# Optimization experiments

Hardware: AMD Instinct MI355X
Metric: run time of the kernel (lower is better)

The kernel has to match this reference:

```python
import jax, jax.numpy as jnp
import numpy as np

ROUTING_ITERS = 3
EPS = 1e-8


def squash(x):
    # scale = ||x||^2 / (1 + ||x||^2); out = scale * x / (||x|| + eps)
    norm = jnp.linalg.norm(x, axis=-1, keepdims=True)
    scale = norm ** 2 / (1.0 + norm ** 2)
    return scale * x / (norm + EPS)


def setup_inputs() -> dict:
    key = jax.random.key(0)
    kx, kw = jax.random.split(key)
    B, R, C, IC, OC = 256, 1152, 10, 8, 16
    x = jax.random.normal(kx, (B, R, IC), dtype=jnp.float32)
    # learned prediction weights: [1, num_routes, num_capsules, in_ch, out_ch]
    weights = jax.random.normal(kw, (1, R, C, IC, OC), dtype=jnp.float32)
    return {"x": x, "weights": weights}


def reference(x, weights):
    # prediction vectors u_hat[b,r,c,o] = sum_i x[b,r,i] * W[r,c,i,o]
    u = jnp.einsum('bri,rcio->brco', x, weights[0])  # [B,R,C,OC]
    b = jnp.zeros(u.shape[:3], dtype=u.dtype)        # routing logits [B,R,C]
    v = jnp.zeros(u.shape[:1] + u.shape[2:], dtype=u.dtype)
    for _ in range(ROUTING_ITERS):
        c = jax.nn.softmax(b, axis=-1)               # coupling coeffs over capsules
        s = jnp.einsum('brc,brco->bco', c, u)        # weighted sum over routes
        v = squash(s)                                # [B,C,OC]
        b = b + jnp.einsum('brco,bco->brc', u, v)    # agreement update
    return v
```

## Files before the change

kernel.cpp:

```cpp
#include <hip/hip_runtime.h>
#include <cstdint>
#include <cstddef>

#define NB 256
#define NR 1152
#define NC 10
#define NI 8
#define NO 16
#define NSPLIT 2
#define NSWEEP 9
#define NRC 144

static __device__ __forceinline__ uint32_t bf16_pack2(float lo, float hi) {
    uint32_t vl = __float_as_uint(lo);
    vl = vl + 0x7FFFu + ((vl >> 16) & 1u);
    uint32_t vh = __float_as_uint(hi);
    vh = vh + 0x7FFFu + ((vh >> 16) & 1u);
    return (vl >> 16) | (vh & 0xFFFF0000u);
}

__global__ __launch_bounds__(320) void caps_u_s1_kernel(
    const float* __restrict__ x, const float* __restrict__ W,
    uint32_t* __restrict__ u, uint32_t* __restrict__ part1)
{
    const int t  = threadIdx.x;
    const int c  = t >> 5;
    const int rl = (t & 31) >> 2;
    const int oq = t & 3;
    const int rc = blockIdx.x >> 4;
    const int bg = blockIdx.x & 15;
    const int b0 = bg * 16;
    const int r  = rc * 8 + rl;

    __shared__ float xs[16][8][8];

    if (t < 256) {
        const int bi = t >> 4, rem = t & 15;
        const int rr = rem >> 1, hf = rem & 1;
        *(float4*)&xs[bi][rr][hf * 4] =
            *(const float4*)(x + ((size_t)(b0 + bi) * NR + rc * 8 + rr) * 8 + hf * 4);
    }

    const float* wb = W + ((size_t)r * NC + c) * (NI * NO) + oq * 4;
    float4 wf[8];
#pragma unroll
    for (int i = 0; i < 8; ++i) wf[i] = *(const float4*)(wb + i * NO);

    __syncthreads();

#pragma unroll 2
    for (int bi = 0; bi < 16; ++bi) {
        const float4 xv4a = *(const float4*)&xs[bi][rl][0];
        const float4 xv4b = *(const float4*)&xs[bi][rl][4];
        const float xr[8] = {xv4a.x, xv4a.y, xv4a.z, xv4a.w,
                             xv4b.x, xv4b.y, xv4b.z, xv4b.w};
        float ax = 0.f, ay = 0.f, az = 0.f, aw = 0.f;
#pragma unroll
        for (int i = 0; i < 8; ++i) {
            const float xv = xr[i];
            ax = fmaf(xv, wf[i].x, ax); ay = fmaf(xv, wf[i].y, ay);
            az = fmaf(xv, wf[i].z, az); aw = fmaf(xv, wf[i].w, aw);
        }
        uint2 s;
        s.x = bf16_pack2(ax, ay);
        s.y = bf16_pack2(az, aw);
        *(uint2*)(u + (((size_t)(b0 + bi) * NC + c) * NR + r) * 8 + oq * 2) = s;

        float sx = ax, sy = ay, sz = az, sw = aw;
#pragma unroll
        for (int off = 4; off <= 16; off <<= 1) {
            sx += __shfl_xor(sx, off); sy += __shfl_xor(sy, off);
            sz += __shfl_xor(sz, off); sw += __shfl_xor(sw, off);
        }
        if ((t & 28) == 0) {
            uint2 p;
            p.x = bf16_pack2(sx, sy);
            p.y = bf16_pack2(sz, sw);
            *(uint2*)(part1 + ((size_t)(b0 + bi) * NRC + rc) * 80
                      + c * 8 + oq * 2) = p;
        }
    }
}

__global__ __launch_bounds__(192) void caps_s1_reduce_kernel(
    const uint32_t* __restrict__ part1, float* __restrict__ vsum)
{
    const int b = blockIdx.x;
    const int t = threadIdx.x;
    if (t >= 160) return;
    const uint32_t* p = part1 + (size_t)b * NRC * 80 + (t >> 1);
    const bool hi = t & 1;
    float s0 = 0.f, s1 = 0.f, s2 = 0.f, s3 = 0.f;
#pragma unroll 4
    for (int g = 0; g < NRC; g += 4) {
        const uint32_t w0 = p[(g + 0) * 80];
        const uint32_t w1 = p[(g + 1) * 80];
        const uint32_t w2 = p[(g + 2) * 80];
        const uint32_t w3 = p[(g + 3) * 80];
        s0 += hi ? __uint_as_float(w0 & 0xFFFF0000u) : __uint_as_float(w0 << 16);
        s1 += hi ? __uint_as_float(w1 & 0xFFFF0000u) : __uint_as_float(w1 << 16);
        s2 += hi ? __uint_as_float(w2 & 0xFFFF0000u) : __uint_as_float(w2 << 16);
        s3 += hi ? __uint_as_float(w3 & 0xFFFF0000u) : __uint_as_float(w3 << 16);
    }
    const float s = 0.1f * ((s0 + s1) + (s2 + s3));
    float n2 = s * s;
    n2 += __shfl_xor(n2, 1);
    n2 += __shfl_xor(n2, 2);
    n2 += __shfl_xor(n2, 4);
    n2 += __shfl_xor(n2, 8);
    const float nrm = sqrtf(n2);
    vsum[(size_t)b * 160 + t] = s * (n2 / (1.f + n2) / (nrm + 1e-8f));
}

__global__ __launch_bounds__(256, 2) void caps_pass_kernel(
    const uint32_t* __restrict__ u, const float* __restrict__ vsum,
    const float* __restrict__ part_prev, float* __restrict__ partout)
{
    const int b  = blockIdx.x >> 1;
    const int sp = blockIdx.x & 1;
    const int t  = threadIdx.x;
    const int oq = t & 3;
    const int rl = t >> 2;

    __shared__ float vss[160];
    __shared__ float sred[4][160];

    if (t < 160) {
        float v = vsum[(size_t)b * 160 + t];
        if (part_prev != nullptr) {
            const float s = part_prev[(size_t)b * 160 + t]
                          + part_prev[((size_t)NB + b) * 160 + t];
            float n2 = s * s;
            n2 += __shfl_xor(n2, 1);
            n2 += __shfl_xor(n2, 2);
            n2 += __shfl_xor(n2, 4);
            n2 += __shfl_xor(n2, 8);
            const float nrm = sqrtf(n2);
            v += s * (n2 / (1.f + n2) / (nrm + 1e-8f));
        }
        vss[t] = v;
    }
    __syncthreads();

    float acc[10][4];
#pragma unroll
    for (int c = 0; c < 10; ++c)
#pragma unroll
        for (int j = 0; j < 4; ++j) acc[c][j] = 0.f;

    const uint2* ub = (const uint2*)u + (size_t)b * NC * NR * 4 + oq;

    for (int k = 0; k < NSWEEP; ++k) {
        const int r = sp * (NSWEEP * 64) + k * 64 + rl;
        uint2 q[10];
#pragma unroll
        for (int c = 0; c < 10; ++c) q[c] = ub[((size_t)c * NR + r) * 4];

        float lg[10];
#pragma unroll
        for (int c = 0; c < 10; ++c) {
            const float4 vq = *(const float4*)&vss[c * 16 + oq * 4];
            float d = __uint_as_float(q[c].x << 16) * vq.x;
            d = fmaf(__uint_as_float(q[c].x & 0xFFFF0000u), vq.y, d);
            d = fmaf(__uint_as_float(q[c].y << 16),         vq.z, d);
            d = fmaf(__uint_as_float(q[c].y & 0xFFFF0000u), vq.w, d);
            lg[c] = d;
        }
#pragma unroll
        for (int c = 0; c < 10; ++c) {
            lg[c] += __shfl_xor(lg[c], 1);
            lg[c] += __shfl_xor(lg[c], 2);
        }
        float m = lg[0];
#pragma unroll
        for (int c = 1; c < 10; ++c) m = fmaxf(m, lg[c]);
        float wgt[10], ssum = 0.f;
#pragma unroll
        for (int c = 0; c < 10; ++c) { wgt[c] = __expf(lg[c] - m); ssum += wgt[c]; }
        const float inv = 1.f / ssum;
#pragma unroll
        for (int c = 0; c < 10; ++c) {
            const float wv = wgt[c] * inv;
            acc[c][0] = fmaf(wv, __uint_as_float(q[c].x << 16),         acc[c][0]);
            acc[c][1] = fmaf(wv, __uint_as_float(q[c].x & 0xFFFF0000u), acc[c][1]);
            acc[c][2] = fmaf(wv, __uint_as_float(q[c].y << 16),         acc[c][2]);
            acc[c][3] = fmaf(wv, __uint_as_float(q[c].y & 0xFFFF0000u), acc[c][3]);
        }
    }

#pragma unroll
    for (int off = 4; off <= 32; off <<= 1)
#pragma unroll
        for (int c = 0; c < 10; ++c)
#pragma unroll
            for (int j = 0; j < 4; ++j) acc[c][j] += __shfl_xor(acc[c][j], off);

    const int wv = t >> 6;
    if ((t & 63) < 4) {
#pragma unroll
        for (int c = 0; c < 10; ++c)
#pragma unroll
            for (int j = 0; j < 4; ++j)
                sred[wv][c * 16 + oq * 4 + j] = acc[c][j];
    }
    __syncthreads();

    if (t < 160) {
        partout[((size_t)sp * NB + b) * 160 + t]
            = sred[0][t] + sred[1][t] + sred[2][t] + sred[3][t];
    }
}

__global__ __launch_bounds__(192) void caps_final_kernel(
    const float* __restrict__ p2b, float* __restrict__ out)
{
    const int b = blockIdx.x;
    const int t = threadIdx.x;
    if (t >= 160) return;
    const float s = p2b[(size_t)b * 160 + t]
                  + p2b[((size_t)NB + b) * 160 + t];
    float n2 = s * s;
    n2 += __shfl_xor(n2, 1);
    n2 += __shfl_xor(n2, 2);
    n2 += __shfl_xor(n2, 4);
    n2 += __shfl_xor(n2, 8);
    const float nrm   = sqrtf(n2);
    const float scale = n2 / (1.f + n2) / (nrm + 1e-8f);
    out[(size_t)b * 160 + t] = scale * s;
}

extern "C" void kernel_launch(void* const* d_in, const int* in_sizes, int n_in,
                              void* d_out, int out_size, void* d_ws, size_t ws_size,
                              hipStream_t stream) {
    const float* x = (const float*)d_in[0];
    const float* W = (const float*)d_in[1];
    float* out = (float*)d_out;

    uint8_t*  ws   = (uint8_t*)d_ws;
    uint32_t* u    = (uint32_t*)ws;
    uint32_t* prt1 = (uint32_t*)(ws + 94371840u);
    float*    p2a  = (float*)(ws + 94371840u + 11796480u);
    float*    p2b  = (float*)(ws + 94371840u + 11796480u + 327680u);
    float*    vsm  = (float*)(ws + 94371840u + 11796480u + 655360u);

    caps_u_s1_kernel     <<<2304, 320, 0, stream>>>(x, W, u, prt1);
    caps_s1_reduce_kernel<<<NB, 192, 0, stream>>>(prt1, vsm);
    caps_pass_kernel     <<<NB * NSPLIT, 256, 0, stream>>>(u, vsm, nullptr, p2a);
    caps_pass_kernel     <<<NB * NSPLIT, 256, 0, stream>>>(u, vsm, p2a, p2b);
    caps_final_kernel    <<<NB, 192, 0, stream>>>(p2b, out);
}
```

Before: 139.4 us.

## Recompute prediction vectors on the fly from fp16 x and W instead of storing u

The first kernel no longer writes the full bf16 u tensor (about 94 MB). It writes fp16 copies of x and W instead. Each routing pass recomputes u[b,r,c,:] from those copies with packed fp16 dot2 instructions, replacing the large u read with small x and W reads, of which W is shared across batches and likely cached. In exchange it adds ALU work in every pass, uses fp16 with round-toward-zero conversion for the recomputed u, and raises register pressure from the us[10][4] array.

```diff
diff --git a/kernel.cpp b/kernel.cpp
--- a/kernel.cpp
+++ b/kernel.cpp
@@ -11,6 +11,38 @@
 #define NSWEEP 9
 #define NRC 144
 
+typedef _Float16 h2 __attribute__((ext_vector_type(2)));
+
+#if defined(__has_builtin)
+#if __has_builtin(__builtin_amdgcn_fdot2)
+#define HAS_FDOT2 1
+#endif
+#if __has_builtin(__builtin_amdgcn_cvt_pkrtz)
+#define HAS_PKRTZ 1
+#endif
+#endif
+
+static __device__ __forceinline__ float fdot2(uint32_t a, uint32_t b, float c) {
+#ifdef HAS_FDOT2
+    return __builtin_amdgcn_fdot2(__builtin_bit_cast(h2, a),
+                                  __builtin_bit_cast(h2, b), c, false);
+#else
+    const h2 av = __builtin_bit_cast(h2, a);
+    const h2 bv = __builtin_bit_cast(h2, b);
+    c = fmaf((float)av.x, (float)bv.x, c);
+    return fmaf((float)av.y, (float)bv.y, c);
+#endif
+}
+
+static __device__ __forceinline__ uint32_t pk_f16(float a, float b) {
+#ifdef HAS_PKRTZ
+    return __builtin_bit_cast(uint32_t, __builtin_amdgcn_cvt_pkrtz(a, b));
+#else
+    h2 v; v.x = (_Float16)a; v.y = (_Float16)b;
+    return __builtin_bit_cast(uint32_t, v);
+#endif
+}
+
 static __device__ __forceinline__ uint32_t bf16_pack2(float lo, float hi) {
     uint32_t vl = __float_as_uint(lo);
     vl = vl + 0x7FFFu + ((vl >> 16) & 1u);
@@ -19,9 +51,10 @@
     return (vl >> 16) | (vh & 0xFFFF0000u);
 }
 
-__global__ __launch_bounds__(320) void caps_u_s1_kernel(
+__global__ __launch_bounds__(320) void caps_s1cvt_kernel(
     const float* __restrict__ x, const float* __restrict__ W,
-    uint32_t* __restrict__ u, uint32_t* __restrict__ part1)
+    uint32_t* __restrict__ part1, uint32_t* __restrict__ xf16,
+    uint32_t* __restrict__ wf16)
 {
     const int t  = threadIdx.x;
     const int c  = t >> 5;
@@ -37,14 +70,33 @@
     if (t < 256) {
         const int bi = t >> 4, rem = t & 15;
         const int rr = rem >> 1, hf = rem & 1;
-        *(float4*)&xs[bi][rr][hf * 4] =
+        const float4 xv =
             *(const float4*)(x + ((size_t)(b0 + bi) * NR + rc * 8 + rr) * 8 + hf * 4);
+        *(float4*)&xs[bi][rr][hf * 4] = xv;
+        uint2 xp;
+        xp.x = pk_f16(xv.x, xv.y);
+        xp.y = pk_f16(xv.z, xv.w);
+        *(uint2*)(xf16 + ((size_t)(b0 + bi) * NR + rc * 8 + rr) * 4 + hf * 2) = xp;
     }
 
     const float* wb = W + ((size_t)r * NC + c) * (NI * NO) + oq * 4;
     float4 wf[8];
 #pragma unroll
     for (int i = 0; i < 8; ++i) wf[i] = *(const float4*)(wb + i * NO);
+
+    if (bg == 0) {
+        const float* wfl = (const float*)wf;
+        uint32_t* dst = wf16 + (((size_t)r * NC + c) * 4 + oq) * 16;
+#pragma unroll
+        for (int od = 0; od < 4; ++od) {
+            uint4 wq;
+            wq.x = pk_f16(wfl[0 * 4 + od], wfl[1 * 4 + od]);
+            wq.y = pk_f16(wfl[2 * 4 + od], wfl[3 * 4 + od]);
+            wq.z = pk_f16(wfl[4 * 4 + od], wfl[5 * 4 + od]);
+            wq.w = pk_f16(wfl[6 * 4 + od], wfl[7 * 4 + od]);
+            *(uint4*)(dst + od * 4) = wq;
+        }
+    }
 
     __syncthreads();
 
@@ -61,11 +113,6 @@
             ax = fmaf(xv, wf[i].x, ax); ay = fmaf(xv, wf[i].y, ay);
             az = fmaf(xv, wf[i].z, az); aw = fmaf(xv, wf[i].w, aw);
         }
-        uint2 s;
-        s.x = bf16_pack2(ax, ay);
-        s.y = bf16_pack2(az, aw);
-        *(uint2*)(u + (((size_t)(b0 + bi) * NC + c) * NR + r) * 8 + oq * 2) = s;
-
         float sx = ax, sy = ay, sz = az, sw = aw;
 #pragma unroll
         for (int off = 4; off <= 16; off <<= 1) {
@@ -112,9 +159,10 @@
     vsum[(size_t)b * 160 + t] = s * (n2 / (1.f + n2) / (nrm + 1e-8f));
 }
 
-__global__ __launch_bounds__(256, 2) void caps_pass_kernel(
-    const uint32_t* __restrict__ u, const float* __restrict__ vsum,
-    const float* __restrict__ part_prev, float* __restrict__ partout)
+__global__ __launch_bounds__(256, 2) void caps_pass_f16_kernel(
+    const uint32_t* __restrict__ xf16, const uint32_t* __restrict__ wf16,
+    const float* __restrict__ vsum, const float* __restrict__ part_prev,
+    float* __restrict__ partout)
 {
     const int b  = blockIdx.x >> 1;
     const int sp = blockIdx.x & 1;
@@ -148,22 +196,39 @@
 #pragma unroll
         for (int j = 0; j < 4; ++j) acc[c][j] = 0.f;
 
-    const uint2* ub = (const uint2*)u + (size_t)b * NC * NR * 4 + oq;
-
     for (int k = 0; k < NSWEEP; ++k) {
         const int r = sp * (NSWEEP * 64) + k * 64 + rl;
-        uint2 q[10];
-#pragma unroll
-        for (int c = 0; c < 10; ++c) q[c] = ub[((size_t)c * NR + r) * 4];
-
+        const uint4 xv = *(const uint4*)(xf16 + ((size_t)b * NR + r) * 4);
+
+        float us[10][4];
         float lg[10];
 #pragma unroll
         for (int c = 0; c < 10; ++c) {
+            const uint4* wp =
+                (const uint4*)(wf16 + (((size_t)r * NC + c) * 4 + oq) * 16);
+            const uint4 w0 = wp[0], w1 = wp[1], w2 = wp[2], w3 = wp[3];
+            float u0 = fdot2(xv.x, w0.x, 0.f);
+            u0 = fdot2(xv.y, w0.y, u0);
+            u0 = fdot2(xv.z, w0.z, u0);
+            u0 = fdot2(xv.w, w0.w, u0);
+            float u1 = fdot2(xv.x, w1.x, 0.f);
+            u1 = fdot2(xv.y, w1.y, u1);
+            u1 = fdot2(xv.z, w1.z, u1);
+            u1 = fdot2(xv.w, w1.w, u1);
+            float u2 = fdot2(xv.x, w2.x, 0.f);
+            u2 = fdot2(xv.y, w2.y, u2);
+            u2 = fdot2(xv.z, w2.z, u2);
+            u2 = fdot2(xv.w, w2.w, u2);
+            float u3 = fdot2(xv.x, w3.x, 0.f);
+            u3 = fdot2(xv.y, w3.y, u3);
+            u3 = fdot2(xv.z, w3.z, u3);
+            u3 = fdot2(xv.w, w3.w, u3);
+            us[c][0] = u0; us[c][1] = u1; us[c][2] = u2; us[c][3] = u3;
             const float4 vq = *(const float4*)&vss[c * 16 + oq * 4];
-            float d = __uint_as_float(q[c].x << 16) * vq.x;
-            d = fmaf(__uint_as_float(q[c].x & 0xFFFF0000u), vq.y, d);
-            d = fmaf(__uint_as_float(q[c].y << 16),         vq.z, d);
-            d = fmaf(__uint_as_float(q[c].y & 0xFFFF0000u), vq.w, d);
+            float d = u0 * vq.x;
+            d = fmaf(u1, vq.y, d);
+            d = fmaf(u2, vq.z, d);
+            d = fmaf(u3, vq.w, d);
             lg[c] = d;
         }
 #pragma unroll
@@ -181,10 +246,10 @@
 #pragma unroll
         for (int c = 0; c < 10; ++c) {
             const float wv = wgt[c] * inv;
-            acc[c][0] = fmaf(wv, __uint_as_float(q[c].x << 16),         acc[c][0]);
-            acc[c][1] = fmaf(wv, __uint_as_float(q[c].x & 0xFFFF0000u), acc[c][1]);
-            acc[c][2] = fmaf(wv, __uint_as_float(q[c].y << 16),         acc[c][2]);
-            acc[c][3] = fmaf(wv, __uint_as_float(q[c].y & 0xFFFF0000u), acc[c][3]);
+            acc[c][0] = fmaf(wv, us[c][0], acc[c][0]);
+            acc[c][1] = fmaf(wv, us[c][1], acc[c][1]);
+            acc[c][2] = fmaf(wv, us[c][2], acc[c][2]);
+            acc[c][3] = fmaf(wv, us[c][3], acc[c][3]);
         }
     }
 
@@ -237,15 +302,16 @@
     float* out = (float*)d_out;
 
     uint8_t*  ws   = (uint8_t*)d_ws;
-    uint32_t* u    = (uint32_t*)ws;
-    uint32_t* prt1 = (uint32_t*)(ws + 94371840u);
-    float*    p2a  = (float*)(ws + 94371840u + 11796480u);
-    float*    p2b  = (float*)(ws + 94371840u + 11796480u + 327680u);
-    float*    vsm  = (float*)(ws + 94371840u + 11796480u + 655360u);
-
-    caps_u_s1_kernel     <<<2304, 320, 0, stream>>>(x, W, u, prt1);
+    uint32_t* prt1 = (uint32_t*)ws;
+    uint32_t* xf16 = (uint32_t*)(ws + 11796480u);
+    uint32_t* wf16 = (uint32_t*)(ws + 11796480u + 4718592u);
+    float*    p2a  = (float*)(ws + 11796480u + 4718592u + 2949120u);
+    float*    p2b  = (float*)(ws + 11796480u + 4718592u + 2949120u + 327680u);
+    float*    vsm  = (float*)(ws + 11796480u + 4718592u + 2949120u + 655360u);
+
+    caps_s1cvt_kernel    <<<2304, 320, 0, stream>>>(x, W, prt1, xf16, wf16);
     caps_s1_reduce_kernel<<<NB, 192, 0, stream>>>(prt1, vsm);
-    caps_pass_kernel     <<<NB * NSPLIT, 256, 0, stream>>>(u, vsm, nullptr, p2a);
-    caps_pass_kernel     <<<NB * NSPLIT, 256, 0, stream>>>(u, vsm, p2a, p2b);
+    caps_pass_f16_kernel <<<NB * NSPLIT, 256, 0, stream>>>(xf16, wf16, vsm, nullptr, p2a);
+    caps_pass_f16_kernel <<<NB * NSPLIT, 256, 0, stream>>>(xf16, wf16, vsm, p2a, p2b);
     caps_final_kernel    <<<NB, 192, 0, stream>>>(p2b, out);
 }
```

After: 195.2 us. 40.1% more time.
